# Kernel tuning notes

Measured on AMD Instinct MI355X. Metric: run time of the kernel, lower is better.

The kernel has to match this reference:

```python
import jax, jax.numpy as jnp
import numpy as np

K = 32  # sae_k

def setup_inputs() -> dict:
    key = jax.random.key(0)
    k1, k2, k3 = jax.random.split(key, 3)
    B, D, H = 8192, 256, 8192  # batch, d_in, hidden_dim = d_in * scale_size
    x = jax.random.normal(k1, (B, D), dtype=jnp.float32)
    W_enc = jax.random.normal(k2, (H, D), dtype=jnp.float32) * (1.0 / np.sqrt(D))
    b_enc = jnp.zeros((H,), dtype=jnp.float32)
    # W_dec initialized as clone of encoder weight then row-normalized to unit norm
    W_dec = jax.random.normal(k3, (H, D), dtype=jnp.float32)
    W_dec = W_dec / (jnp.linalg.norm(W_dec, axis=1, keepdims=True) + jnp.finfo(jnp.float32).eps)
    b_dec = jnp.zeros((D,), dtype=jnp.float32)
    return {"x": x, "W_enc": W_enc, "b_enc": b_enc, "W_dec": W_dec, "b_dec": b_dec}

def reference(x, W_enc, b_enc, W_dec, b_dec):
    # sae_in = x - b_dec; pre_acts = relu(encoder(sae_in))
    sae_in = x - b_dec
    pre_acts = jax.nn.relu(jnp.einsum('bd,hd->bh', sae_in, W_enc) + b_enc)  # [B, H]
    # top-k activation: keep k largest latents per row, zero the rest
    topk_vals, topk_idx = jax.lax.top_k(pre_acts, K)  # [B, K]
    B = pre_acts.shape[0]
    rows = jnp.arange(B)[:, None]
    z = jnp.zeros_like(pre_acts).at[rows, topk_idx].set(topk_vals)  # sparse activation [B, H]
    # decode
    x_reconstructed = jnp.einsum('bh,hd->bd', z, W_dec) + b_dec
    return x_reconstructed
```

## Files before the change

kernel.cpp:

```cpp
#include <hip/hip_runtime.h>

#define DIN   256
#define HID   8192
#define BATCH 8192
#define TOPK  32
#define BM    64
#define HHALF 4096
#define NCH   16
#define NS1   48
#define MRG   96
#define NS2   48
#define AS_LD 264
#define XF_LD 260
#define CAP   112
#define K2_LD 113
#define WCAP  640
#define THRM  0.1375f
#define DBM   4
#define DT    256
#define GK_OFF ((size_t)4 << 20)

typedef __bf16 bf16x8 __attribute__((ext_vector_type(8)));
typedef unsigned short u16x8 __attribute__((ext_vector_type(8)));
typedef float f32x4v __attribute__((ext_vector_type(4)));

__device__ __forceinline__ unsigned short f2bf(float f) {
  unsigned x = __builtin_bit_cast(unsigned, f);
  x = x + 0x7fffu + ((x >> 16) & 1u);
  return (unsigned short)(x >> 16);
}

__global__ __launch_bounds__(512) void wenc_cast(
    const float* __restrict__ Wenc, unsigned short* __restrict__ wsb)
{
  const int g = (int)blockIdx.x * 512 + (int)threadIdx.x;
  const int h = g >> 5, u = g & 31, kg = u >> 2, quad = u & 3;
  const float* src = Wenc + (size_t)h * DIN + kg * 32 + quad * 8;
  float4 a = *(const float4*)src;
  float4 b = *(const float4*)(src + 4);
  u16x8 o;
  o[0] = f2bf(a.x); o[1] = f2bf(a.y); o[2] = f2bf(a.z); o[3] = f2bf(a.w);
  o[4] = f2bf(b.x); o[5] = f2bf(b.y); o[6] = f2bf(b.z); o[7] = f2bf(b.w);
  *(u16x8*)(wsb + ((size_t)(((h >> 4) * 8 + kg) * 64 + quad * 16 + (h & 15))) * 8) = o;
}

__global__ __launch_bounds__(512) void sae_enc(
    const float* __restrict__ x,    const float* __restrict__ benc,
    const float* __restrict__ bdec, const unsigned short* __restrict__ wsb,
    unsigned* __restrict__ gkeys)
{
  __shared__ __align__(16) union UA {
    unsigned short As[BM][AS_LD];
    struct { unsigned wkey[8][WCAP]; unsigned char wrow[8][WCAP]; } w;
  } ua;
  __shared__ unsigned keys2[BM][K2_LD];
  __shared__ int   cnt[BM];
  __shared__ float rthr[BM];
  __shared__ int   wn[8];

  const int tid  = (int)threadIdx.x;
  const int wave = tid >> 6;
  const int lane = tid & 63;
  const int quad = lane >> 4;
  const int ln15 = lane & 15;
  const int rt   = (int)blockIdx.x >> 1;
  const int hs   = (int)blockIdx.x & 1;
  const int mb   = rt * BM;

  #pragma unroll
  for (int u = 0; u < 2; ++u) {
    const int idx = u * 512 + tid;
    const int r = idx >> 4, seg = idx & 15;
    const float* xs = x + (size_t)(mb + r) * DIN + seg * 16;
    const float* bs = bdec + seg * 16;
    float ss = 0.0f;
    #pragma unroll
    for (int j = 0; j < 4; ++j) {
      float4 xv = *(const float4*)(xs + 4 * j);
      float4 bv = *(const float4*)(bs + 4 * j);
      float dx = xv.x - bv.x, dy = xv.y - bv.y;
      float dz = xv.z - bv.z, dw = xv.w - bv.w;
      ss += dx * dx + dy * dy + dz * dz + dw * dw;
      unsigned short* dst = &ua.As[r][seg * 16 + 4 * j];
      dst[0] = f2bf(dx); dst[1] = f2bf(dy);
      dst[2] = f2bf(dz); dst[3] = f2bf(dw);
    }
    #pragma unroll
    for (int d = 1; d < 16; d <<= 1) ss += __shfl_xor(ss, d, 16);
    if (seg == 0) { rthr[r] = THRM * sqrtf(ss); cnt[r] = 0; }
  }
  __syncthreads();

  bf16x8 afrag[4][8];
  #pragma unroll
  for (int mt = 0; mt < 4; ++mt)
    #pragma unroll
    for (int gk = 0; gk < 8; ++gk)
      afrag[mt][gk] = *(const bf16x8*)&ua.As[mt * 16 + ln15][gk * 32 + quad * 8];

  float thr[16];
  #pragma unroll
  for (int s = 0; s < 16; ++s) thr[s] = rthr[(s >> 2) * 16 + quad * 4 + (s & 3)];
  __syncthreads();

  unsigned wbase = 0;

  for (int c = 0; c < NCH; ++c) {
    const unsigned short* bp =
        wsb + (((size_t)(hs * 256 + c * 16 + wave * 2) * 512) + lane) * 8;
    #pragma unroll
    for (int nt = 0; nt < 2; ++nt) {
      bf16x8 bfrag[8];
      #pragma unroll
      for (int kg = 0; kg < 8; ++kg)
        bfrag[kg] = *(const bf16x8*)(bp + (size_t)nt * 4096 + (size_t)kg * 512);

      const int hcol = hs * HHALF + c * 256 + (wave * 2 + nt) * 16 + ln15;
      const float be = benc[hcol];
      f32x4v acc[4];
      #pragma unroll
      for (int mt = 0; mt < 4; ++mt)
        #pragma unroll
        for (int i = 0; i < 4; ++i) acc[mt][i] = be;

      #pragma unroll
      for (int kg = 0; kg < 8; ++kg)
        #pragma unroll
        for (int mt = 0; mt < 4; ++mt)
          acc[mt] = __builtin_amdgcn_mfma_f32_16x16x32_bf16(
              afrag[mt][kg], bfrag[kg], acc[mt], 0, 0, 0);

      const unsigned idxpart = (unsigned)(8191 - hcol);
      #pragma unroll
      for (int s = 0; s < 16; ++s) {
        const int mt = s >> 2, i = s & 3;
        const bool take = acc[mt][i] > thr[s];
        const unsigned long long bm = __ballot(take);
        if (take) {
          const int pos = (int)wbase + __popcll(bm & ((1ull << lane) - 1ull));
          if (pos < WCAP) {
            ua.w.wkey[wave][pos] = ((unsigned)f2bf(acc[mt][i]) << 16) | idxpart;
            ua.w.wrow[wave][pos] = (unsigned char)(mt * 16 + quad * 4 + i);
          }
        }
        wbase += (unsigned)__popcll(bm);
      }
    }
  }
  if (lane == 0) wn[wave] = (int)(wbase < WCAP ? wbase : WCAP);
  __syncthreads();

  for (int w = 0; w < 8; ++w) {
    const int n = wn[w];
    for (int e = tid; e < n; e += 512) {
      const unsigned k = ua.w.wkey[w][e];
      const int row = (int)ua.w.wrow[w][e];
      const int sl = atomicAdd(&cnt[row], 1);
      if (sl < CAP) keys2[row][sl] = k;
    }
  }
  __syncthreads();

  #pragma unroll
  for (int u = 0; u < 2; ++u) {
    const int row = u * 32 + (tid >> 4), l16 = tid & 15;
    const int n = min(cnt[row], CAP);
    unsigned myk[CAP / 16];
    int rk[CAP / 16];
    #pragma unroll
    for (int j = 0; j < CAP / 16; ++j) {
      const int idx = l16 + 16 * j;
      myk[j] = (idx < n) ? keys2[row][idx] : 0u;
      rk[j] = 0;
    }
    for (int e = 0; e < n; ++e) {
      const unsigned k2 = keys2[row][e];
      #pragma unroll
      for (int j = 0; j < CAP / 16; ++j) rk[j] += (k2 > myk[j]) ? 1 : 0;
    }
    unsigned* gout = gkeys + (size_t)(mb + row) * MRG + hs * NS1;
    #pragma unroll
    for (int j = 0; j < CAP / 16; ++j) {
      const int idx = l16 + 16 * j;
      if (idx < n && rk[j] < NS1) gout[rk[j]] = myk[j];
    }
    if (l16 == 0)
      for (int p = n; p < NS1; ++p) gout[p] = (unsigned)(0x4000 + hs * 64 + p);
  }
}

__global__ __launch_bounds__(DT) void sae_dec(
    const float* __restrict__ x,    const float* __restrict__ Wenc,
    const float* __restrict__ benc, const float* __restrict__ Wdec,
    const float* __restrict__ bdec, const unsigned* __restrict__ gkeys,
    float* __restrict__ out)
{
  __shared__ unsigned mk[DBM][MRG];
  __shared__ __align__(16) float xf[DBM][XF_LD];
  __shared__ float tv[DBM][NS2];
  __shared__ int   ti[DBM][NS2];
  __shared__ float sv[DBM][TOPK];
  __shared__ int   si[DBM][TOPK];

  const int tid = (int)threadIdx.x;
  const int mb  = (int)blockIdx.x * DBM;

  #pragma unroll
  for (int i = tid; i < DBM * MRG; i += DT)
    mk[i / MRG][i % MRG] = gkeys[(size_t)mb * MRG + i];

  {
    const int r = tid >> 6, seg = tid & 63;
    float4 xv = *(const float4*)(x + (size_t)(mb + r) * DIN + seg * 4);
    float4 bv = *(const float4*)(bdec + seg * 4);
    float4 d;
    d.x = xv.x - bv.x; d.y = xv.y - bv.y; d.z = xv.z - bv.z; d.w = xv.w - bv.w;
    *(float4*)&xf[r][seg * 4] = d;
  }
  __syncthreads();

  if (tid < DBM * 16) {
    const int row = tid >> 4, l16 = tid & 15;
    unsigned myk[6];
    int rk[6];
    #pragma unroll
    for (int j = 0; j < 6; ++j) {
      myk[j] = mk[row][l16 + 16 * j];
      rk[j]  = 0;
    }
    for (int e = 0; e < MRG; ++e) {
      unsigned k2 = mk[row][e];
      #pragma unroll
      for (int j = 0; j < 6; ++j) rk[j] += (k2 > myk[j]) ? 1 : 0;
    }
    #pragma unroll
    for (int j = 0; j < 6; ++j)
      if (rk[j] < NS2) ti[row][rk[j]] = 8191 - (int)(myk[j] & 0xFFFFu);
  }
  __syncthreads();

  {
    const int sub = tid & 3, pidx = tid >> 2;
    #pragma unroll
    for (int j = 0; j < (DBM * NS2 * 4) / DT; ++j) {
      const int pp = j * (DT / 4) + pidx;
      const int row = pp / NS2, cand = pp - row * NS2;
      const int h = ti[row][cand];
      double a0 = 0.0, a1 = 0.0;
      if (h >= 0) {
        const float* wp = Wenc + (size_t)h * DIN + sub * 64;
        const float* xp = &xf[row][sub * 64];
        #pragma unroll
        for (int kk = 0; kk < 16; ++kk) {
          float4 w  = *(const float4*)(wp + 4 * kk);
          float4 xv = *(const float4*)(xp + 4 * kk);
          a0 += (double)xv.x * (double)w.x + (double)xv.y * (double)w.y;
          a1 += (double)xv.z * (double)w.z + (double)xv.w * (double)w.w;
        }
      }
      double accd = a0 + a1;
      accd += __shfl_down(accd, 2, 4);
      accd += __shfl_down(accd, 1, 4);
      if (sub == 0) {
        float ev = (h >= 0) ? ((float)accd + benc[h]) : 0.0f;
        ev = ev > 0.0f ? ev : 0.0f;
        tv[row][cand] = ev;
      }
    }
  }
  __syncthreads();

  if (tid < DBM * NS2) {
    const int row = tid / NS2, cand = tid - row * NS2;
    const float v = tv[row][cand];
    const int   h = ti[row][cand];
    int rk = 0;
    for (int e = 0; e < NS2; ++e) {
      const float v2 = tv[row][e];
      const int   h2 = ti[row][e];
      rk += (v2 > v || (v2 == v && (unsigned)h2 < (unsigned)h)) ? 1 : 0;
    }
    if (rk < TOPK) { sv[row][rk] = v; si[row][rk] = h; }
  }
  __syncthreads();

  {
    const int r = tid >> 6, d0 = (tid & 63) * 4;
    float4 bb = *(const float4*)(bdec + d0);
    float o0 = bb.x, o1 = bb.y, o2 = bb.z, o3 = bb.w;
    #pragma unroll
    for (int s = 0; s < TOPK; ++s) {
      const float v = sv[r][s];
      const int   h = si[r][s];
      const float* wp = Wdec + (size_t)((v > 0.0f) ? h : 0) * DIN + d0;
      float4 w = *(const float4*)wp;
      o0 += v * w.x; o1 += v * w.y; o2 += v * w.z; o3 += v * w.w;
    }
    float4 o;
    o.x = o0; o.y = o1; o.z = o2; o.w = o3;
    *(float4*)(out + (size_t)(mb + r) * DIN + d0) = o;
  }
}

extern "C" void kernel_launch(void* const* d_in, const int* in_sizes, int n_in,
                              void* d_out, int out_size, void* d_ws, size_t ws_size,
                              hipStream_t stream) {
  const float* x    = (const float*)d_in[0];
  const float* Wenc = (const float*)d_in[1];
  const float* benc = (const float*)d_in[2];
  const float* Wdec = (const float*)d_in[3];
  const float* bdec = (const float*)d_in[4];
  float* out = (float*)d_out;
  unsigned short* wsb = (unsigned short*)d_ws;
  unsigned* gkeys = (unsigned*)((char*)d_ws + GK_OFF);

  wenc_cast<<<dim3((HID * DIN / 8) / 512), dim3(512), 0, stream>>>(Wenc, wsb);
  sae_enc<<<dim3(2 * BATCH / BM), dim3(512), 0, stream>>>(x, benc, bdec, wsb, gkeys);
  sae_dec<<<dim3(BATCH / DBM), dim3(DT), 0, stream>>>(x, Wenc, benc, Wdec, bdec, gkeys, out);
}
```

Measured before the change: 242.1 us.

## Shrink rescore candidate set and batch weight loads in decode kernel

Reduces the number of candidates re-scored in exact precision per row from 48 to 40, which cuts the fp64 encoder dot products and Wenc row gathers in the decode kernel. The candidate-ranking step now uses 32 threads per row with 3 keys each instead of 16 threads with 6. The Wenc and Wdec loads are issued as batches before the FMAs so more memory requests are in flight, and launch bounds are raised for occupancy. Fewer rescored candidates raises the risk that a true top-k latent is missed when the approximate bf16 scores misorder near the cutoff.

```diff
diff --git a/kernel.cpp b/kernel.cpp
--- a/kernel.cpp
+++ b/kernel.cpp
@@ -9,7 +9,7 @@
 #define NCH   16
 #define NS1   48
 #define MRG   96
-#define NS2   48
+#define NS2   40
 #define AS_LD 264
 #define XF_LD 260
 #define CAP   112
@@ -189,7 +189,7 @@
   }
 }
 
-__global__ __launch_bounds__(DT) void sae_dec(
+__global__ __launch_bounds__(DT, 4) void sae_dec(
     const float* __restrict__ x,    const float* __restrict__ Wenc,
     const float* __restrict__ benc, const float* __restrict__ Wdec,
     const float* __restrict__ bdec, const unsigned* __restrict__ gkeys,
@@ -219,43 +219,40 @@
   }
   __syncthreads();
 
-  if (tid < DBM * 16) {
-    const int row = tid >> 4, l16 = tid & 15;
-    unsigned myk[6];
-    int rk[6];
-    #pragma unroll
-    for (int j = 0; j < 6; ++j) {
-      myk[j] = mk[row][l16 + 16 * j];
-      rk[j]  = 0;
-    }
+  if (tid < DBM * 32) {
+    const int row = tid >> 5, l32 = tid & 31;
+    unsigned myk[3];
+    int rk[3];
+    #pragma unroll
+    for (int j = 0; j < 3; ++j) { myk[j] = mk[row][l32 + 32 * j]; rk[j] = 0; }
     for (int e = 0; e < MRG; ++e) {
-      unsigned k2 = mk[row][e];
-      #pragma unroll
-      for (int j = 0; j < 6; ++j) rk[j] += (k2 > myk[j]) ? 1 : 0;
-    }
-    #pragma unroll
-    for (int j = 0; j < 6; ++j)
+      const unsigned k2 = mk[row][e];
+      #pragma unroll
+      for (int j = 0; j < 3; ++j) rk[j] += (k2 > myk[j]) ? 1 : 0;
+    }
+    #pragma unroll
+    for (int j = 0; j < 3; ++j)
       if (rk[j] < NS2) ti[row][rk[j]] = 8191 - (int)(myk[j] & 0xFFFFu);
   }
   __syncthreads();
 
   {
     const int sub = tid & 3, pidx = tid >> 2;
-    #pragma unroll
-    for (int j = 0; j < (DBM * NS2 * 4) / DT; ++j) {
-      const int pp = j * (DT / 4) + pidx;
+    for (int pp = pidx; pp < DBM * NS2; pp += DT / 4) {
       const int row = pp / NS2, cand = pp - row * NS2;
       const int h = ti[row][cand];
       double a0 = 0.0, a1 = 0.0;
       if (h >= 0) {
         const float* wp = Wenc + (size_t)h * DIN + sub * 64;
         const float* xp = &xf[row][sub * 64];
+        float4 w[16];
+        #pragma unroll
+        for (int kk = 0; kk < 16; ++kk) w[kk] = *(const float4*)(wp + 4 * kk);
         #pragma unroll
         for (int kk = 0; kk < 16; ++kk) {
-          float4 w  = *(const float4*)(wp + 4 * kk);
           float4 xv = *(const float4*)(xp + 4 * kk);
-          a0 += (double)xv.x * (double)w.x + (double)xv.y * (double)w.y;
-          a1 += (double)xv.z * (double)w.z + (double)xv.w * (double)w.w;
+          a0 += (double)xv.x * (double)w[kk].x + (double)xv.y * (double)w[kk].y;
+          a1 += (double)xv.z * (double)w[kk].z + (double)xv.w * (double)w[kk].w;
         }
       }
       double accd = a0 + a1;
@@ -289,12 +286,19 @@
     float4 bb = *(const float4*)(bdec + d0);
     float o0 = bb.x, o1 = bb.y, o2 = bb.z, o3 = bb.w;
     #pragma unroll
-    for (int s = 0; s < TOPK; ++s) {
-      const float v = sv[r][s];
-      const int   h = si[r][s];
-      const float* wp = Wdec + (size_t)((v > 0.0f) ? h : 0) * DIN + d0;
-      float4 w = *(const float4*)wp;
-      o0 += v * w.x; o1 += v * w.y; o2 += v * w.z; o3 += v * w.w;
+    for (int sc = 0; sc < TOPK; sc += 8) {
+      float vv[8]; int hh[8];
+      #pragma unroll
+      for (int q = 0; q < 8; ++q) { vv[q] = sv[r][sc + q]; hh[q] = si[r][sc + q]; }
+      float4 w[8];
+      #pragma unroll
+      for (int q = 0; q < 8; ++q)
+        w[q] = *(const float4*)(Wdec + (size_t)((vv[q] > 0.0f) ? hh[q] : 0) * DIN + d0);
+      #pragma unroll
+      for (int q = 0; q < 8; ++q) {
+        o0 += vv[q] * w[q].x; o1 += vv[q] * w[q].y;
+        o2 += vv[q] * w[q].z; o3 += vv[q] * w[q].w;
+      }
     }
     float4 o;
     o.x = o0; o.y = o1; o.z = o2; o.w = o3;
```

New measurement: 252.0 us. +4.1%, slower.
